# Kernel optimization log

Measured on AMD Instinct MI355X. Metric: run time of the kernel, lower is better.

## Reference

```python
import jax, jax.numpy as jnp
import numpy as np

N_NODES = 100000

def setup_inputs() -> dict:
    key = jax.random.key(0)
    k1, k2, k3, k4, k5, k6 = jax.random.split(key, 6)
    n_edges = 1000000
    in_feat, out_feat = 64, 64
    return {
        "h_src": jax.random.normal(k1, (N_NODES, in_feat), dtype=jnp.float32),
        "h_dst": jax.random.normal(k2, (N_NODES, in_feat), dtype=jnp.float32),
        "src": jax.random.randint(k3, (n_edges,), 0, N_NODES, dtype=jnp.int64),
        "dst": jax.random.randint(k4, (n_edges,), 0, N_NODES, dtype=jnp.int64),
        "weight": jax.random.normal(k5, (out_feat, 2 * in_feat), dtype=jnp.float32) * 0.1,
        "bias": jax.random.normal(k6, (out_feat,), dtype=jnp.float32) * 0.1,
    }

def reference(h_src, h_dst, src, dst, weight, bias):
    # gather messages from source nodes along edges: [E, F]
    msgs = h_src[src]
    # scatter-sum into destination nodes, then divide by in-degree -> mean
    summed = jax.ops.segment_sum(msgs, dst, num_segments=N_NODES)  # [N, F]
    deg = jax.ops.segment_sum(jnp.ones((dst.shape[0],), dtype=h_src.dtype), dst,
                              num_segments=N_NODES)  # [N]
    h_N = summed / jnp.maximum(deg, 1.0)[:, None]
    # concat self + neighbor mean, then linear (torch layout: y = x @ W.T + b)
    h_total = jnp.concatenate([h_dst, h_N], axis=1)  # [N, 2F]
    return h_total @ weight.T + bias
```

## Files before the change

### kernel.cpp

```cpp
#include <hip/hip_runtime.h>
#include <hip/hip_bf16.h>
#include <hip/hip_fp16.h>

#define N_NODES_C 100000
#define NSCAN     102400
#define NBKT      256
#define NBLK      512

union U2H { unsigned u; __half2 h; };

typedef _Float16 h2v __attribute__((ext_vector_type(2)));
typedef __fp16   p2v __attribute__((ext_vector_type(2)));
union U2HV { unsigned u; h2v h; };
union U2PV { unsigned u; p2v p; };

__device__ __forceinline__ __half2 addp(__half2 a, unsigned u)
{
    U2H c; c.u = u;
    return __hadd2(a, c.h);
}

__device__ __forceinline__ __half2 shfl_xor_h2(__half2 v, int m)
{
    U2H c; c.h = v;
    c.u = (unsigned)__shfl_xor((int)c.u, m, 64);
    return c.h;
}

__device__ __forceinline__ float dot2(unsigned xu, unsigned wu, float c)
{
#if __has_builtin(__builtin_amdgcn_fdot2)
    U2HV a, b;
    a.u = xu; b.u = wu;
    return __builtin_amdgcn_fdot2(a.h, b.h, c, false);
#else
    asm("v_dot2_f32_f16 %0, %1, %2, %0" : "+v"(c) : "v"(xu), "v"(wu));
    return c;
#endif
}

__device__ __forceinline__ uint4 pk8(float4 f0, float4 f1)
{
    U2PV a, b, c, d;
    a.p = __builtin_amdgcn_cvt_pkrtz(f0.x, f0.y);
    b.p = __builtin_amdgcn_cvt_pkrtz(f0.z, f0.w);
    c.p = __builtin_amdgcn_cvt_pkrtz(f1.x, f1.y);
    d.p = __builtin_amdgcn_cvt_pkrtz(f1.z, f1.w);
    return make_uint4(a.u, b.u, c.u, d.u);
}

__global__ __launch_bounds__(256) void convert_fp16(
    const float* __restrict__ x, uint4* __restrict__ y, int n8)
{
    int i = blockIdx.x * 256 + threadIdx.x;
    if (i >= n8 + 8) return;
    if (i >= n8) { y[i] = make_uint4(0u, 0u, 0u, 0u); return; }
    const float4* x4 = reinterpret_cast<const float4*>(x);
    float4 a = x4[i * 2 + 0];
    float4 b = x4[i * 2 + 1];
    U2H c0, c1, c2, c3;
    c0.h = __floats2half2_rn(a.x, a.y);
    c1.h = __floats2half2_rn(a.z, a.w);
    c2.h = __floats2half2_rn(b.x, b.y);
    c3.h = __floats2half2_rn(b.z, b.w);
    uint4 o;
    o.x = c0.u; o.y = c1.u; o.z = c2.u; o.w = c3.u;
    y[i] = o;
}

__global__ __launch_bounds__(256) void partA0(
    const int* __restrict__ dst, int* __restrict__ bucket_hist, int n_edges)
{
    __shared__ int h[NBKT];
    int t = threadIdx.x;
    h[t] = 0;
    __syncthreads();
    int chunk = (n_edges + NBLK - 1) / NBLK;
    int start = blockIdx.x * chunk;
    int end   = min(start + chunk, n_edges);
    for (int e = start + t; e < end; e += 256)
        atomicAdd(&h[dst[e] >> 9], 1);
    __syncthreads();
    int c = h[t];
    if (c) atomicAdd(&bucket_hist[t], c);
}

__global__ __launch_bounds__(256) void partA1(
    const int* __restrict__ bucket_hist, int* __restrict__ bucket_base,
    int* __restrict__ cursor, int n_edges)
{
    int t = threadIdx.x;
    int v = bucket_hist[t];
    int incl = v;
    #pragma unroll
    for (int off = 1; off < 64; off <<= 1) {
        int u = __shfl_up(incl, off, 64);
        if ((t & 63) >= off) incl += u;
    }
    __shared__ int wsum[4];
    if ((t & 63) == 63) wsum[t >> 6] = incl;
    __syncthreads();
    int add = 0;
    for (int w = 0; w < (t >> 6); ++w) add += wsum[w];
    incl += add;
    int excl = incl - v;
    bucket_base[t] = excl;
    cursor[t] = excl;
    if (t == 255) bucket_base[256] = incl;
}

__global__ __launch_bounds__(256) void partA2(
    const int* __restrict__ src, const int* __restrict__ dst,
    int* __restrict__ cursor, int* __restrict__ packed, int n_edges)
{
    __shared__ int h[NBKT];
    __shared__ int lcur[NBKT];
    int t = threadIdx.x;
    h[t] = 0;
    __syncthreads();
    int chunk = (n_edges + NBLK - 1) / NBLK;
    int start = blockIdx.x * chunk;
    int end   = min(start + chunk, n_edges);
    for (int e = start + t; e < end; e += 256)
        atomicAdd(&h[dst[e] >> 9], 1);
    __syncthreads();
    int c = h[t];
    int base = 0;
    if (c) base = atomicAdd(&cursor[t], c);
    lcur[t] = base;
    __syncthreads();
    for (int e = start + t; e < end; e += 256) {
        int d = dst[e];
        int pos = atomicAdd(&lcur[d >> 9], 1);
        packed[pos] = (src[e] << 9) | (d & 511);
    }
}

__global__ __launch_bounds__(256) void partB(
    const int* __restrict__ packed, const int* __restrict__ bucket_base,
    int* __restrict__ offsets, int* __restrict__ edge_src)
{
    __shared__ int cnt[512];
    __shared__ int sA[512], sB[512];
    int t = threadIdx.x;
    int k = blockIdx.x;
    int b0 = bucket_base[k];
    int b1 = bucket_base[k + 1];

    cnt[t] = 0; cnt[t + 256] = 0;
    __syncthreads();
    for (int i = b0 + t; i < b1; i += 256)
        atomicAdd(&cnt[packed[i] & 511], 1);
    __syncthreads();

    sA[t] = cnt[t]; sA[t + 256] = cnt[t + 256];
    __syncthreads();
    int* pin  = sA;
    int* pout = sB;
    for (int off = 1; off < 512; off <<= 1) {
        int a = pin[t];
        if (t >= off) a += pin[t - off];
        int b = pin[t + 256] + pin[t + 256 - off];
        pout[t] = a; pout[t + 256] = b;
        __syncthreads();
        int* tmp = pin; pin = pout; pout = tmp;
    }

    {
        int j0 = t, j1 = t + 256;
        int e0 = pin[j0] - cnt[j0];
        int e1 = pin[j1] - cnt[j1];
        int d0 = k * 512 + j0;
        int d1 = k * 512 + j1;
        offsets[d0] = b0 + e0;
        offsets[d1] = b0 + e1;
        cnt[j0] = b0 + e0;
        cnt[j1] = b0 + e1;
    }
    __syncthreads();

    for (int i = b0 + t; i < b1; i += 256) {
        int p = packed[i];
        int pos = atomicAdd(&cnt[p & 511], 1);
        edge_src[pos] = p >> 9;
    }
}

__global__ __launch_bounds__(256) void sage_gather(
    const uint4* __restrict__ hsb,
    const int*   __restrict__ offsets,
    const int*   __restrict__ edge_src,
    uint4*       __restrict__ meanh,
    int n_nodes)
{
    int wid  = (blockIdx.x * 256 + threadIdx.x) >> 6;
    int lane = threadIdx.x & 63;
    int slot = lane >> 3;
    int chunk = lane & 7;

    int e0  = offsets[wid];
    int e1  = offsets[wid + 1];
    int deg = e1 - e0;
    int nit = (deg + 7) >> 3;

    __half2 a0, a1, a2, a3;
    {
        U2H z; z.u = 0u;
        a0 = z.h; a1 = z.h; a2 = z.h; a3 = z.h;
    }

    for (int it = 0; it < nit; ++it) {
        int idx = e0 + (it << 3) + slot;
        int s = (idx < e1) ? edge_src[idx] : N_NODES_C;
        uint4 v = hsb[(size_t)s * 8 + chunk];
        a0 = addp(a0, v.x);
        a1 = addp(a1, v.y);
        a2 = addp(a2, v.z);
        a3 = addp(a3, v.w);
    }

    #pragma unroll
    for (int m = 8; m < 64; m <<= 1) {
        a0 = __hadd2(a0, shfl_xor_h2(a0, m));
        a1 = __hadd2(a1, shfl_xor_h2(a1, m));
        a2 = __hadd2(a2, shfl_xor_h2(a2, m));
        a3 = __hadd2(a3, shfl_xor_h2(a3, m));
    }

    if (lane < 8) {
        float invd = 1.0f / (float)(deg > 1 ? deg : 1);
        U2H o0, o1, o2, o3;
        o0.h = __floats2half2_rn(__low2float(a0) * invd, __high2float(a0) * invd);
        o1.h = __floats2half2_rn(__low2float(a1) * invd, __high2float(a1) * invd);
        o2.h = __floats2half2_rn(__low2float(a2) * invd, __high2float(a2) * invd);
        o3.h = __floats2half2_rn(__low2float(a3) * invd, __high2float(a3) * invd);
        meanh[(size_t)wid * 8 + lane] = make_uint4(o0.u, o1.u, o2.u, o3.u);
    }
}

__global__ __launch_bounds__(256) void sage_gemm(
    const float* __restrict__ h_dst,
    const uint4* __restrict__ meanh,
    const float* __restrict__ weight,
    const float* __restrict__ bias,
    float*       __restrict__ out,
    int n_nodes)
{
    __shared__ uint4 xh4[64 * 16];
    __shared__ uint4 wh4[64 * 16];

    const int t    = threadIdx.x;
    const int base = blockIdx.x * 64;

    const float4* w4g = reinterpret_cast<const float4*>(weight);
    const float4* hd4 = reinterpret_cast<const float4*>(h_dst);

    #pragma unroll
    for (int q = 0; q < 4; ++q) {
        int idx = t + q * 256;
        int o   = idx >> 4;
        int c4  = idx & 15;
        float4 f0 = w4g[o * 32 + c4 * 2 + 0];
        float4 f1 = w4g[o * 32 + c4 * 2 + 1];
        wh4[o * 16 + ((c4 + (o >> 2)) & 15)] = pk8(f0, f1);
    }

    #pragma unroll
    for (int q = 0; q < 2; ++q) {
        int idx = t + q * 256;
        int r   = idx >> 3;
        int c4  = idx & 7;
        int g   = base + r;
        float4 f0 = make_float4(0.f, 0.f, 0.f, 0.f);
        float4 f1 = f0;
        if (g < n_nodes) {
            f0 = hd4[(size_t)g * 16 + c4 * 2 + 0];
            f1 = hd4[(size_t)g * 16 + c4 * 2 + 1];
        }
        xh4[r * 16 + ((c4 + r) & 15)] = pk8(f0, f1);
    }

    #pragma unroll
    for (int q = 0; q < 2; ++q) {
        int idx = t + q * 256;
        int r   = idx >> 3;
        int c8  = idx & 7;
        int g   = base + r;
        uint4 mv = make_uint4(0u, 0u, 0u, 0u);
        if (g < n_nodes)
            mv = meanh[(size_t)g * 8 + c8];
        xh4[r * 16 + (((8 + c8) + r) & 15)] = mv;
    }
    __syncthreads();

    const int m  = t & 15;
    const int r0 = t >> 4;
    const int o0 = m * 4;

    float4 bv = reinterpret_cast<const float4*>(bias)[m];

    float acc[4][4];
    #pragma unroll
    for (int i = 0; i < 4; ++i) {
        acc[i][0] = bv.x; acc[i][1] = bv.y; acc[i][2] = bv.z; acc[i][3] = bv.w;
    }

    #pragma unroll 4
    for (int c4 = 0; c4 < 16; ++c4) {
        uint4 wq[4];
        #pragma unroll
        for (int jj = 0; jj < 4; ++jj) {
            int o = o0 + jj;
            wq[jj] = wh4[o * 16 + ((c4 + m) & 15)];
        }
        #pragma unroll
        for (int i = 0; i < 4; ++i) {
            int r = r0 + 16 * i;
            uint4 xq = xh4[r * 16 + ((c4 + r) & 15)];
            #pragma unroll
            for (int jj = 0; jj < 4; ++jj) {
                float a = acc[i][jj];
                a = dot2(xq.x, wq[jj].x, a);
                a = dot2(xq.y, wq[jj].y, a);
                a = dot2(xq.z, wq[jj].z, a);
                a = dot2(xq.w, wq[jj].w, a);
                acc[i][jj] = a;
            }
        }
    }

    #pragma unroll
    for (int i = 0; i < 4; ++i) {
        int g = base + r0 + 16 * i;
        if (g < n_nodes) {
            float4 ov = make_float4(acc[i][0], acc[i][1], acc[i][2], acc[i][3]);
            reinterpret_cast<float4*>(out)[(size_t)g * 16 + m] = ov;
        }
    }
}

extern "C" void kernel_launch(void* const* d_in, const int* in_sizes, int n_in,
                              void* d_out, int out_size, void* d_ws, size_t ws_size,
                              hipStream_t stream)
{
    const float* h_src  = (const float*)d_in[0];
    const float* h_dst  = (const float*)d_in[1];
    const int*   src    = (const int*)d_in[2];
    const int*   dst    = (const int*)d_in[3];
    const float* weight = (const float*)d_in[4];
    const float* bias   = (const float*)d_in[5];
    float*       out    = (float*)d_out;

    const int n_edges = in_sizes[2];
    const int n_feat  = in_sizes[0];

    int*   bucket_hist = (int*)d_ws;
    int*   bucket_base = bucket_hist + 256;
    int*   cursor      = bucket_base + 260;
    int*   packed      = cursor + 256;
    int*   edge_src    = packed + n_edges;
    uint4* hsb         = (uint4*)(edge_src + n_edges + 64);
    uint4* meanh       = hsb + (size_t)(N_NODES_C + 1) * 8;
    int*   offsets     = (int*)(meanh + (size_t)N_NODES_C * 8);

    hipMemsetAsync(bucket_hist, 0, 256 * sizeof(int), stream);

    int n8 = n_feat / 8;
    convert_fp16<<<(n8 + 8 + 255) / 256, 256, 0, stream>>>(h_src, hsb, n8);

    partA0<<<NBLK, 256, 0, stream>>>(dst, bucket_hist, n_edges);
    partA1<<<1, 256, 0, stream>>>(bucket_hist, bucket_base, cursor, n_edges);
    partA2<<<NBLK, 256, 0, stream>>>(src, dst, cursor, packed, n_edges);
    partB<<<(N_NODES_C + 511) / 512, 256, 0, stream>>>(
        packed, bucket_base, offsets, edge_src);

    sage_gather<<<N_NODES_C / 4, 256, 0, stream>>>(
        hsb, offsets, edge_src, meanh, N_NODES_C);

    sage_gemm<<<(N_NODES_C + 63) / 64, 256, 0, stream>>>(
        h_dst, meanh, weight, bias, out, N_NODES_C);
}
```

Before: 128.3 us.

## Fuse fp16 conversion with histogram, use per-block bucket offsets instead of atomics

```diff
diff --git a/kernel.cpp b/kernel.cpp
--- a/kernel.cpp
+++ b/kernel.cpp
@@ -49,48 +49,50 @@
     return make_uint4(a.u, b.u, c.u, d.u);
 }
 
-__global__ __launch_bounds__(256) void convert_fp16(
-    const float* __restrict__ x, uint4* __restrict__ y, int n8)
-{
-    int i = blockIdx.x * 256 + threadIdx.x;
-    if (i >= n8 + 8) return;
-    if (i >= n8) { y[i] = make_uint4(0u, 0u, 0u, 0u); return; }
-    const float4* x4 = reinterpret_cast<const float4*>(x);
-    float4 a = x4[i * 2 + 0];
-    float4 b = x4[i * 2 + 1];
-    U2H c0, c1, c2, c3;
-    c0.h = __floats2half2_rn(a.x, a.y);
-    c1.h = __floats2half2_rn(a.z, a.w);
-    c2.h = __floats2half2_rn(b.x, b.y);
-    c3.h = __floats2half2_rn(b.z, b.w);
-    uint4 o;
-    o.x = c0.u; o.y = c1.u; o.z = c2.u; o.w = c3.u;
-    y[i] = o;
-}
-
-__global__ __launch_bounds__(256) void partA0(
-    const int* __restrict__ dst, int* __restrict__ bucket_hist, int n_edges)
+__global__ __launch_bounds__(256) void fusedA0(
+    const float* __restrict__ x, uint4* __restrict__ y, int n8,
+    const int* __restrict__ dst, int* __restrict__ bucket_cnt, int n_edges,
+    int nConv)
 {
     __shared__ int h[NBKT];
     int t = threadIdx.x;
-    h[t] = 0;
-    __syncthreads();
-    int chunk = (n_edges + NBLK - 1) / NBLK;
-    int start = blockIdx.x * chunk;
-    int end   = min(start + chunk, n_edges);
-    for (int e = start + t; e < end; e += 256)
-        atomicAdd(&h[dst[e] >> 9], 1);
-    __syncthreads();
-    int c = h[t];
-    if (c) atomicAdd(&bucket_hist[t], c);
-}
-
-__global__ __launch_bounds__(256) void partA1(
-    const int* __restrict__ bucket_hist, int* __restrict__ bucket_base,
-    int* __restrict__ cursor, int n_edges)
+    if ((int)blockIdx.x < nConv) {
+        int i = blockIdx.x * 256 + t;
+        if (i >= n8 + 8) return;
+        if (i >= n8) { y[i] = make_uint4(0u, 0u, 0u, 0u); return; }
+        const float4* x4 = reinterpret_cast<const float4*>(x);
+        float4 a = x4[i * 2 + 0];
+        float4 b = x4[i * 2 + 1];
+        U2H c0, c1, c2, c3;
+        c0.h = __floats2half2_rn(a.x, a.y);
+        c1.h = __floats2half2_rn(a.z, a.w);
+        c2.h = __floats2half2_rn(b.x, b.y);
+        c3.h = __floats2half2_rn(b.z, b.w);
+        uint4 o;
+        o.x = c0.u; o.y = c1.u; o.z = c2.u; o.w = c3.u;
+        y[i] = o;
+    } else {
+        int blk = blockIdx.x - nConv;
+        h[t] = 0;
+        __syncthreads();
+        int chunk = (n_edges + NBLK - 1) / NBLK;
+        int start = blk * chunk;
+        int end   = min(start + chunk, n_edges);
+        for (int e = start + t; e < end; e += 256)
+            atomicAdd(&h[dst[e] >> 9], 1);
+        __syncthreads();
+        bucket_cnt[blk * NBKT + t] = h[t];
+    }
+}
+
+__global__ __launch_bounds__(256) void partA1a(
+    const int* __restrict__ bucket_cnt, int* __restrict__ bucket_base)
 {
     int t = threadIdx.x;
-    int v = bucket_hist[t];
+    int v = 0;
+    #pragma unroll 8
+    for (int blk = 0; blk < NBLK; ++blk)
+        v += bucket_cnt[blk * NBKT + t];
     int incl = v;
     #pragma unroll
     for (int off = 1; off < 64; off <<= 1) {
@@ -103,32 +105,50 @@
     int add = 0;
     for (int w = 0; w < (t >> 6); ++w) add += wsum[w];
     incl += add;
-    int excl = incl - v;
-    bucket_base[t] = excl;
-    cursor[t] = excl;
+    bucket_base[t] = incl - v;
     if (t == 255) bucket_base[256] = incl;
+}
+
+__global__ __launch_bounds__(256) void partA1b(
+    const int* __restrict__ bucket_cnt, const int* __restrict__ bucket_base,
+    int* __restrict__ blk_base)
+{
+    __shared__ int c[512];
+    __shared__ int sA[512], sB[512];
+    int t = threadIdx.x;
+    int b = blockIdx.x;
+    c[t]       = bucket_cnt[t * NBKT + b];
+    c[t + 256] = bucket_cnt[(t + 256) * NBKT + b];
+    __syncthreads();
+    sA[t] = c[t]; sA[t + 256] = c[t + 256];
+    __syncthreads();
+    int* pin  = sA;
+    int* pout = sB;
+    for (int off = 1; off < 512; off <<= 1) {
+        int a0 = pin[t];
+        if (t >= off) a0 += pin[t - off];
+        int a1 = pin[t + 256] + pin[t + 256 - off];
+        pout[t] = a0; pout[t + 256] = a1;
+        __syncthreads();
+        int* tmp = pin; pin = pout; pout = tmp;
+    }
+    int base = bucket_base[b];
+    blk_base[b * NBLK + t]       = base + pin[t] - c[t];
+    blk_base[b * NBLK + t + 256] = base + pin[t + 256] - c[t + 256];
 }
 
 __global__ __launch_bounds__(256) void partA2(
     const int* __restrict__ src, const int* __restrict__ dst,
-    int* __restrict__ cursor, int* __restrict__ packed, int n_edges)
-{
-    __shared__ int h[NBKT];
+    const int* __restrict__ blk_base, int* __restrict__ packed, int n_edges)
+{
     __shared__ int lcur[NBKT];
     int t = threadIdx.x;
-    h[t] = 0;
+    int blk = blockIdx.x;
+    lcur[t] = blk_base[t * NBLK + blk];
     __syncthreads();
     int chunk = (n_edges + NBLK - 1) / NBLK;
-    int start = blockIdx.x * chunk;
+    int start = blk * chunk;
     int end   = min(start + chunk, n_edges);
-    for (int e = start + t; e < end; e += 256)
-        atomicAdd(&h[dst[e] >> 9], 1);
-    __syncthreads();
-    int c = h[t];
-    int base = 0;
-    if (c) base = atomicAdd(&cursor[t], c);
-    lcur[t] = base;
-    __syncthreads();
     for (int e = start + t; e < end; e += 256) {
         int d = dst[e];
         int pos = atomicAdd(&lcur[d >> 9], 1);
@@ -170,10 +190,8 @@
         int j0 = t, j1 = t + 256;
         int e0 = pin[j0] - cnt[j0];
         int e1 = pin[j1] - cnt[j1];
-        int d0 = k * 512 + j0;
-        int d1 = k * 512 + j1;
-        offsets[d0] = b0 + e0;
-        offsets[d1] = b0 + e1;
+        offsets[k * 512 + j0] = b0 + e0;
+        offsets[k * 512 + j1] = b0 + e1;
         cnt[j0] = b0 + e0;
         cnt[j1] = b0 + e1;
     }
@@ -354,23 +372,23 @@
     const int n_edges = in_sizes[2];
     const int n_feat  = in_sizes[0];
 
-    int*   bucket_hist = (int*)d_ws;
-    int*   bucket_base = bucket_hist + 256;
-    int*   cursor      = bucket_base + 260;
-    int*   packed      = cursor + 256;
+    int*   bucket_cnt  = (int*)d_ws;
+    int*   blk_base    = bucket_cnt + NBLK * NBKT;
+    int*   bucket_base = blk_base + NBKT * NBLK;
+    int*   packed      = bucket_base + 260;
     int*   edge_src    = packed + n_edges;
     uint4* hsb         = (uint4*)(edge_src + n_edges + 64);
     uint4* meanh       = hsb + (size_t)(N_NODES_C + 1) * 8;
     int*   offsets     = (int*)(meanh + (size_t)N_NODES_C * 8);
 
-    hipMemsetAsync(bucket_hist, 0, 256 * sizeof(int), stream);
-
     int n8 = n_feat / 8;
-    convert_fp16<<<(n8 + 8 + 255) / 256, 256, 0, stream>>>(h_src, hsb, n8);
-
-    partA0<<<NBLK, 256, 0, stream>>>(dst, bucket_hist, n_edges);
-    partA1<<<1, 256, 0, stream>>>(bucket_hist, bucket_base, cursor, n_edges);
-    partA2<<<NBLK, 256, 0, stream>>>(src, dst, cursor, packed, n_edges);
+    int nConv = (n8 + 8 + 255) / 256;
+
+    fusedA0<<<nConv + NBLK, 256, 0, stream>>>(
+        h_src, hsb, n8, dst, bucket_cnt, n_edges, nConv);
+    partA1a<<<1, 256, 0, stream>>>(bucket_cnt, bucket_base);
+    partA1b<<<NBKT, 256, 0, stream>>>(bucket_cnt, bucket_base, blk_base);
+    partA2<<<NBLK, 256, 0, stream>>>(src, dst, blk_base, packed, n_edges);
     partB<<<(N_NODES_C + 511) / 512, 256, 0, stream>>>(
         packed, bucket_base, offsets, edge_src);
 
```

Measured after the change: 117.8 us. -8.2%, faster.
